# Kernel optimization log

Hardware: AMD Instinct MI355X
Metric: run time of the kernel (lower is better)

## Reference

```python
import jax, jax.numpy as jnp
import numpy as np

B, T, D, L = 16, 2048, 1024, 4


def setup_inputs() -> dict:
    key = jax.random.key(0)
    k1, k2, k3 = jax.random.split(key, 3)
    x = jax.random.normal(k1, (B, T, D), dtype=jnp.float32)
    lengths = jax.random.randint(k2, (B,), 1, T + 1, dtype=jnp.int32)
    s = float(np.sqrt(3.0 / D))  # SRU uniform init range
    W = jax.random.uniform(k3, (L, D, 3 * D), dtype=jnp.float32, minval=-s, maxval=s)
    b = jnp.zeros((L, 2 * D), dtype=jnp.float32)
    return {"x": x, "lengths": lengths, "W": W, "b": b}


def _sru_layer(h, W_l, b_l):
    # h: [T, B, D]; W_l: [D, 3D]; b_l: [2D]
    U = jnp.einsum('tbd,de->tbe', h, W_l)            # [T, B, 3D]
    x_tilde, zf, zr = jnp.split(U, 3, axis=-1)
    f = jax.nn.sigmoid(zf + b_l[:D])                 # forget gate
    r = jax.nn.sigmoid(zr + b_l[D:])                 # reset/highway gate

    def step(c, fx):
        f_t, x_t = fx
        c_new = f_t * c + (1.0 - f_t) * x_t          # c_t = f*c_{t-1} + (1-f)*x~
        return c_new, c_new

    c0 = jnp.zeros(h.shape[1:], dtype=h.dtype)       # [B, D]
    _, c_seq = jax.lax.scan(step, c0, (f, x_tilde))  # [T, B, D]
    # v1 + has_skip_term, n_in == n_out: highway over raw input
    return r * jnp.tanh(c_seq) + (1.0 - r) * h


def reference(x, lengths, W, b):
    # x: [B, T, D] -> [T, B, D] (module permutes before SRU)
    h = jnp.transpose(x, (1, 0, 2))
    for l in range(L):  # fixed small layer count
        h = _sru_layer(h, W[l], b[l])
    h = jnp.transpose(h, (1, 0, 2))                  # [B, T, D]
    # _select_last: pick h[i, lengths[i]-1]
    return h[jnp.arange(B), lengths - 1]             # [B, D]
```

## Files before the change

kernel.cpp:

```cpp
#include <hip/hip_runtime.h>


typedef float f32x4 __attribute__((ext_vector_type(4)));
typedef int   i32x4 __attribute__((ext_vector_type(4)));
typedef char  c8x4  __attribute__((ext_vector_type(4)));
typedef _Float16 f16;

#define SRU_B 16
#define SRU_T 2048
#define SRU_D 1024
#define SRU_L 4
#define SRU_N 3072
#define SPAN 256

#define A_SCALE 4096.0f
#define W_SCALE 2048.0f
#define Z2_INV  1.1920928955078125e-7f
#define H_INV   2.44140625e-4f

__device__ __forceinline__ void q16split(float v, float scale, signed char& hi,
                                         signed char& lo) {
  int q = __float2int_rn(v * scale);
  q = min(max(q, -32512), 32512);
  int h = (q + 128) >> 8;
  hi = (signed char)h;
  lo = (signed char)(q - (h << 8));
}

__device__ __forceinline__ void mfma_i8(i32x4& c, i32x4 a, i32x4 b) {
  asm("v_mfma_i32_16x16x64_i8 %0, %1, %2, %0" : "+v"(c) : "v"(a), "v"(b));
}

#define GLDS(g, l) __builtin_amdgcn_global_load_lds(                      \
    (const __attribute__((address_space(1))) void*)(g),                   \
    (__attribute__((address_space(3))) void*)(l), 16, 0, 0)

__global__ void convert_w_kernel(const float* __restrict__ W,
                                 signed char* __restrict__ Wt8) {
  __shared__ float tile[32][33];
  const int l = blockIdx.z;
  const int n0 = blockIdx.x * 32, k0 = blockIdx.y * 32;
  const int tx = threadIdx.x & 31, ty = threadIdx.x >> 5;
  const float* Wl = W + (size_t)l * SRU_D * SRU_N;
#pragma unroll
  for (int i = 0; i < 32; i += 8)
    tile[ty + i][tx] = Wl[(size_t)(k0 + ty + i) * SRU_N + n0 + tx];
  __syncthreads();
  const size_t ob = (size_t)l * SRU_N * SRU_D;
#pragma unroll
  for (int i = 0; i < 32; i += 8) {
    float v = tile[tx][ty + i];
    size_t o = ob + (size_t)(n0 + ty + i) * SRU_D + k0 + tx;
    Wt8[o] = (signed char)__float2int_rn(v * W_SCALE);
  }
}

__global__ void convert_x_kernel(const float* __restrict__ x,
                                 const int* __restrict__ lengths,
                                 signed char* __restrict__ Hh,
                                 signed char* __restrict__ Hl) {
  const size_t i = (size_t)blockIdx.x * 256 + threadIdx.x;
  const int b = (int)(i >> 19), t = (int)((i >> 8) & 2047);
  if (t >= lengths[b]) return;
  f32x4 v = ((const f32x4*)x)[i];
  c8x4 hi, lo;
#pragma unroll
  for (int j = 0; j < 4; ++j) {
    signed char h, l;
    q16split(v[j], A_SCALE, h, l);
    hi[j] = h;
    lo[j] = l;
  }
  ((c8x4*)Hh)[i] = hi;
  ((c8x4*)Hl)[i] = lo;
}

__global__ __launch_bounds__(256, 2) void gemm2_kernel(
    const signed char* __restrict__ Ah, const signed char* __restrict__ Al,
    const signed char* __restrict__ Bq,
    const int* __restrict__ lengths, const float* __restrict__ bias,
    f16* __restrict__ Ux, f16* __restrict__ Uf, f16* __restrict__ Ur,
    int last) {
  const int bn = blockIdx.x, bm = blockIdx.y;
  const int b = bm >> 4, tb = bm & 15;
  const int lenb = lengths[b];
  if (tb * 128 >= lenb) return;
  if (last && bn >= 16) {
    if (((lenb - 1) >> 7) != tb) return;
  }

  __shared__ __align__(16) signed char lAh[16384], lAl[16384], lB[16384];
  const int tid = threadIdx.x;
  const int lane = tid & 63, wid = tid >> 6;
  const int wm = (wid >> 1) * 64, wn = (wid & 1) * 64;
  const int fr = lane & 15;
  const int fko = ((lane >> 4) * 16) ^ (((lane >> 1) & 3) * 16);

  i32x4 acc1[4][4] = {};
  i32x4 acc2[4][4] = {};

  const int sr = tid >> 2;
  const int sc = (((tid & 3) ^ ((tid >> 3) & 3)) * 16);
  const size_t abase = ((size_t)b * SRU_T + tb * 128) * SRU_D;
  const signed char* gAh = Ah + abase + (size_t)sr * 1024 + sc;
  const signed char* gAl = Al + abase + (size_t)sr * 1024 + sc;
  const signed char* gB  = Bq + (size_t)(bn * 128 + sr) * 1024 + sc;

  auto stage = [&](int k0, int bs) {
    const int o = bs * 8192 + wid * 1024;
    GLDS(gAh + k0, &lAh[o]); GLDS(gAh + 65536 + k0, &lAh[o + 4096]);
    GLDS(gAl + k0, &lAl[o]); GLDS(gAl + 65536 + k0, &lAl[o + 4096]);
    GLDS(gB  + k0, &lB[o]);  GLDS(gB  + 65536 + k0, &lB[o + 4096]);
  };

  stage(0, 0);
  __syncthreads();
  int cur = 0;
  for (int step = 0; step < 16; ++step) {
    if (step + 1 < 16) stage((step + 1) * 64, cur ^ 1);
    const int cb = cur * 8192;
    i32x4 ah[4], al[4];
#pragma unroll
    for (int i = 0; i < 4; ++i) {
      const int ro = cb + (wm + i * 16 + fr) * 64 + fko;
      ah[i] = *(const i32x4*)&lAh[ro];
      al[i] = *(const i32x4*)&lAl[ro];
    }
#pragma unroll
    for (int ni = 0; ni < 4; ++ni) {
      const int ro = cb + (wn + ni * 16 + fr) * 64 + fko;
      i32x4 bv = *(const i32x4*)&lB[ro];
#pragma unroll
      for (int mi = 0; mi < 4; ++mi) {
        mfma_i8(acc1[mi][ni], ah[mi], bv);
        mfma_i8(acc2[mi][ni], al[mi], bv);
      }
    }
    __syncthreads();
    cur ^= 1;
  }

  const int urow0 = bm * 128 + wm + (lane >> 4) * 4;
  const int gcol = bn * 128 + wn + fr;
  const int region = gcol >> 10;
  const int d0 = gcol & 1023;
  if (region == 0) {
#pragma unroll
    for (int mi = 0; mi < 4; ++mi)
#pragma unroll
      for (int ni = 0; ni < 4; ++ni)
#pragma unroll
        for (int r = 0; r < 4; ++r) {
          float z = (256.f * (float)acc1[mi][ni][r] +
                     (float)acc2[mi][ni][r]) * Z2_INV;
          Ux[((size_t)(urow0 + mi * 16 + r) << 10) + d0 + ni * 16] = (f16)z;
        }
  } else {
    const float* bp = bias + (region == 2 ? SRU_D : 0);
    float bv[4];
#pragma unroll
    for (int ni = 0; ni < 4; ++ni) bv[ni] = bp[d0 + ni * 16];
    f16* dst = (region == 1) ? Uf : Ur;
#pragma unroll
    for (int mi = 0; mi < 4; ++mi)
#pragma unroll
      for (int ni = 0; ni < 4; ++ni)
#pragma unroll
        for (int r = 0; r < 4; ++r) {
          float z = (256.f * (float)acc1[mi][ni][r] +
                     (float)acc2[mi][ni][r]) * Z2_INV;
          float s = 1.f / (1.f + __expf(-(z + bv[ni])));
          dst[((size_t)(urow0 + mi * 16 + r) << 10) + d0 + ni * 16] = (f16)s;
        }
  }
}

__global__ __launch_bounds__(512) void scan_kernel(
    const f16* __restrict__ Ux, const f16* __restrict__ Uf,
    const f16* __restrict__ Ur,
    const int* __restrict__ lengths,
    signed char* __restrict__ Hh, signed char* __restrict__ Hl, int last) {
  __shared__ float sP[8][64], sL[8][64];
  const int dblk = blockIdx.x, b = blockIdx.y;
  const int lane = threadIdx.x & 63, w = threadIdx.x >> 6;
  const int d = (dblk << 6) + lane;
  const int lenb = lengths[b];
  const int start = w * SPAN;
  const size_t rbase = (((size_t)b * SRU_T + start) << 10) + d;

  float P = 1.f, Lv = 0.f;
  if (start < lenb) {
    const int nbt = (min(SPAN, lenb - start) + 7) >> 3;
    const f16* Xr = Ux + rbase;
    const f16* Fr = Uf + rbase;
    float xt_n[8], ff_n[8];
#pragma unroll
    for (int j = 0; j < 8; ++j) {
      xt_n[j] = (float)Xr[(size_t)j << 10];
      ff_n[j] = (float)Fr[(size_t)j << 10];
    }
    for (int bt = 0; bt < nbt; ++bt) {
      float xt[8], ff[8];
#pragma unroll
      for (int j = 0; j < 8; ++j) { xt[j] = xt_n[j]; ff[j] = ff_n[j]; }
      if (bt + 1 < nbt) {
        const size_t o2 = (size_t)((bt + 1) * 8) << 10;
#pragma unroll
        for (int j = 0; j < 8; ++j) {
          xt_n[j] = (float)Xr[o2 + ((size_t)j << 10)];
          ff_n[j] = (float)Fr[o2 + ((size_t)j << 10)];
        }
      }
#pragma unroll
      for (int j = 0; j < 8; ++j) {
        Lv = ff[j] * Lv + (1.f - ff[j]) * xt[j];
        P *= ff[j];
      }
    }
  }
  sP[w][lane] = P;
  sL[w][lane] = Lv;
  __syncthreads();
  if (start >= lenb) return;

  float c = 0.f;
#pragma unroll
  for (int j = 0; j < 8; ++j)
    if (j < w) c = sP[j][lane] * c + sL[j][lane];

  const int nbt = (min(SPAN, lenb - start) + 7) >> 3;
  const f16* Xr = Ux + rbase;
  const f16* Fr = Uf + rbase;
  const f16* Rr = Ur + rbase;
  signed char* ph = Hh + rbase;
  signed char* pl = Hl + rbase;

  float xt_n[8], ff_n[8], rr_n[8], hv_n[8];
#pragma unroll
  for (int j = 0; j < 8; ++j) {
    xt_n[j] = (float)Xr[(size_t)j << 10];
    ff_n[j] = (float)Fr[(size_t)j << 10];
    rr_n[j] = (float)Rr[(size_t)j << 10];
    hv_n[j] = (float)((int)ph[(size_t)j << 10] * 256 + (int)pl[(size_t)j << 10]) * H_INV;
  }
  for (int bt = 0; bt < nbt; ++bt) {
    float xt[8], ff[8], rr[8], hv[8];
#pragma unroll
    for (int j = 0; j < 8; ++j) {
      xt[j] = xt_n[j]; ff[j] = ff_n[j]; rr[j] = rr_n[j]; hv[j] = hv_n[j];
    }
    if (bt + 1 < nbt) {
      const size_t o2 = (size_t)((bt + 1) * 8) << 10;
#pragma unroll
      for (int j = 0; j < 8; ++j) {
        xt_n[j] = (float)Xr[o2 + ((size_t)j << 10)];
        ff_n[j] = (float)Fr[o2 + ((size_t)j << 10)];
        rr_n[j] = (float)Rr[o2 + ((size_t)j << 10)];
        hv_n[j] = (float)((int)ph[o2 + ((size_t)j << 10)] * 256 +
                          (int)pl[o2 + ((size_t)j << 10)]) * H_INV;
      }
    }
    signed char* wh = ph + ((size_t)(bt * 8) << 10);
    signed char* wl = pl + ((size_t)(bt * 8) << 10);
#pragma unroll
    for (int j = 0; j < 8; ++j) {
      c = ff[j] * c + (1.f - ff[j]) * xt[j];
      const int t = start + bt * 8 + j;
      const bool wr = last ? (t == lenb - 1) : (t < lenb);
      if (wr) {
        float e = __expf(-2.f * fabsf(c));
        float th = copysignf((1.f - e) / (1.f + e), c);
        float o = rr[j] * th + (1.f - rr[j]) * hv[j];
        signed char oh, ol;
        q16split(o, A_SCALE, oh, ol);
        wh[(size_t)j << 10] = oh;
        wl[(size_t)j << 10] = ol;
      }
    }
  }
}

__global__ void select_kernel(const signed char* __restrict__ Hh,
                              const signed char* __restrict__ Hl,
                              const int* __restrict__ lengths,
                              float* __restrict__ out) {
  const int b = blockIdx.x;
  const int t = lengths[b] - 1;
#pragma unroll
  for (int j = 0; j < 4; ++j) {
    int d = threadIdx.x + j * 256;
    size_t idx = (((size_t)b * SRU_T + t) << 10) + d;
    out[(b << 10) + d] = (float)((int)Hh[idx] * 256 + (int)Hl[idx]) * H_INV;
  }
}

extern "C" void kernel_launch(void* const* d_in, const int* in_sizes, int n_in,
                              void* d_out, int out_size, void* d_ws, size_t ws_size,
                              hipStream_t stream) {
  const float* x = (const float*)d_in[0];
  const int* lengths = (const int*)d_in[1];
  const float* W = (const float*)d_in[2];
  const float* bias = (const float*)d_in[3];
  float* out = (float*)d_out;

  char* ws = (char*)d_ws;
  size_t off = 0;
  auto alloc = [&](size_t n) { void* p = ws + off; off += (n + 255) & ~(size_t)255; return p; };
  signed char* Hh  = (signed char*)alloc((size_t)SRU_T * SRU_B * SRU_D);
  signed char* Hl  = (signed char*)alloc((size_t)SRU_T * SRU_B * SRU_D);
  signed char* Wt8 = (signed char*)alloc((size_t)SRU_L * SRU_N * SRU_D);
  f16*   Ux   = (f16*)alloc((size_t)SRU_T * SRU_B * SRU_D * 2);
  f16*   Uf   = (f16*)alloc((size_t)SRU_T * SRU_B * SRU_D * 2);
  f16*   Ur   = (f16*)alloc((size_t)SRU_T * SRU_B * SRU_D * 2);

  hipLaunchKernelGGL(convert_w_kernel, dim3(SRU_N / 32, SRU_D / 32, SRU_L), dim3(256), 0, stream,
                     W, Wt8);
  hipLaunchKernelGGL(convert_x_kernel, dim3((SRU_B * SRU_T * SRU_D / 4) / 256), dim3(256), 0, stream,
                     x, lengths, Hh, Hl);

  for (int l = 0; l < SRU_L; ++l) {
    const signed char* Bq = Wt8 + (size_t)l * SRU_N * SRU_D;
    const float* bl_ = bias + (size_t)l * 2 * SRU_D;
    const int last = (l == SRU_L - 1) ? 1 : 0;
    hipLaunchKernelGGL(gemm2_kernel, dim3(SRU_N / 128, SRU_B * SRU_T / 128), dim3(256), 0, stream,
                       Hh, Hl, Bq, lengths, bl_, Ux, Uf, Ur, last);
    hipLaunchKernelGGL(scan_kernel, dim3(SRU_D / 64, SRU_B), dim3(512), 0, stream,
                       Ux, Uf, Ur, lengths, Hh, Hl, last);
  }
  hipLaunchKernelGGL(select_kernel, dim3(SRU_B), dim3(256), 0, stream, Hh, Hl, lengths, out);
}
```

Measured before the change: 889.0 us.

## Remap GEMM blocks across XCDs and fold final selection into last scan

```diff
diff --git a/kernel.cpp b/kernel.cpp
--- a/kernel.cpp
+++ b/kernel.cpp
@@ -81,13 +81,19 @@
     const int* __restrict__ lengths, const float* __restrict__ bias,
     f16* __restrict__ Ux, f16* __restrict__ Uf, f16* __restrict__ Ur,
     int last) {
-  const int bn = blockIdx.x, bm = blockIdx.y;
-  const int b = bm >> 4, tb = bm & 15;
+  const int id = blockIdx.x;
+  const int xcd = id & 7;
+  const int r = id >> 3;
+  const int bn = r % 24;
+  const int q = r / 24;
+  const int b = q >> 1;
+  const int tb = ((xcd - b) & 7) | ((q & 1) << 3);
   const int lenb = lengths[b];
   if (tb * 128 >= lenb) return;
   if (last && bn >= 16) {
     if (((lenb - 1) >> 7) != tb) return;
   }
+  const int bm = (b << 4) | tb;
 
   __shared__ __align__(16) signed char lAh[16384], lAl[16384], lB[16384];
   const int tid = threadIdx.x;
@@ -150,10 +156,10 @@
 #pragma unroll
       for (int ni = 0; ni < 4; ++ni)
 #pragma unroll
-        for (int r = 0; r < 4; ++r) {
-          float z = (256.f * (float)acc1[mi][ni][r] +
-                     (float)acc2[mi][ni][r]) * Z2_INV;
-          Ux[((size_t)(urow0 + mi * 16 + r) << 10) + d0 + ni * 16] = (f16)z;
+        for (int r2 = 0; r2 < 4; ++r2) {
+          float z = (256.f * (float)acc1[mi][ni][r2] +
+                     (float)acc2[mi][ni][r2]) * Z2_INV;
+          Ux[((size_t)(urow0 + mi * 16 + r2) << 10) + d0 + ni * 16] = (f16)z;
         }
   } else {
     const float* bp = bias + (region == 2 ? SRU_D : 0);
@@ -166,11 +172,11 @@
 #pragma unroll
       for (int ni = 0; ni < 4; ++ni)
 #pragma unroll
-        for (int r = 0; r < 4; ++r) {
-          float z = (256.f * (float)acc1[mi][ni][r] +
-                     (float)acc2[mi][ni][r]) * Z2_INV;
+        for (int r2 = 0; r2 < 4; ++r2) {
+          float z = (256.f * (float)acc1[mi][ni][r2] +
+                     (float)acc2[mi][ni][r2]) * Z2_INV;
           float s = 1.f / (1.f + __expf(-(z + bv[ni])));
-          dst[((size_t)(urow0 + mi * 16 + r) << 10) + d0 + ni * 16] = (f16)s;
+          dst[((size_t)(urow0 + mi * 16 + r2) << 10) + d0 + ni * 16] = (f16)s;
         }
   }
 }
@@ -179,7 +185,8 @@
     const f16* __restrict__ Ux, const f16* __restrict__ Uf,
     const f16* __restrict__ Ur,
     const int* __restrict__ lengths,
-    signed char* __restrict__ Hh, signed char* __restrict__ Hl, int last) {
+    signed char* __restrict__ Hh, signed char* __restrict__ Hl,
+    float* __restrict__ out, int last) {
   __shared__ float sP[8][64], sL[8][64];
   const int dblk = blockIdx.x, b = blockIdx.y;
   const int lane = threadIdx.x & 63, w = threadIdx.x >> 6;
@@ -222,6 +229,7 @@
   sL[w][lane] = Lv;
   __syncthreads();
   if (start >= lenb) return;
+  if (last && (lenb - 1 < start || lenb - 1 >= start + SPAN)) return;
 
   float c = 0.f;
 #pragma unroll
@@ -266,8 +274,13 @@
     for (int j = 0; j < 8; ++j) {
       c = ff[j] * c + (1.f - ff[j]) * xt[j];
       const int t = start + bt * 8 + j;
-      const bool wr = last ? (t == lenb - 1) : (t < lenb);
-      if (wr) {
+      if (last) {
+        if (t == lenb - 1) {
+          float e = __expf(-2.f * fabsf(c));
+          float th = copysignf((1.f - e) / (1.f + e), c);
+          out[(b << 10) + d] = rr[j] * th + (1.f - rr[j]) * hv[j];
+        }
+      } else if (t < lenb) {
         float e = __expf(-2.f * fabsf(c));
         float th = copysignf((1.f - e) / (1.f + e), c);
         float o = rr[j] * th + (1.f - rr[j]) * hv[j];
@@ -277,20 +290,6 @@
         wl[(size_t)j << 10] = ol;
       }
     }
-  }
-}
-
-__global__ void select_kernel(const signed char* __restrict__ Hh,
-                              const signed char* __restrict__ Hl,
-                              const int* __restrict__ lengths,
-                              float* __restrict__ out) {
-  const int b = blockIdx.x;
-  const int t = lengths[b] - 1;
-#pragma unroll
-  for (int j = 0; j < 4; ++j) {
-    int d = threadIdx.x + j * 256;
-    size_t idx = (((size_t)b * SRU_T + t) << 10) + d;
-    out[(b << 10) + d] = (float)((int)Hh[idx] * 256 + (int)Hl[idx]) * H_INV;
   }
 }
 
@@ -322,10 +321,9 @@
     const signed char* Bq = Wt8 + (size_t)l * SRU_N * SRU_D;
     const float* bl_ = bias + (size_t)l * 2 * SRU_D;
     const int last = (l == SRU_L - 1) ? 1 : 0;
-    hipLaunchKernelGGL(gemm2_kernel, dim3(SRU_N / 128, SRU_B * SRU_T / 128), dim3(256), 0, stream,
+    hipLaunchKernelGGL(gemm2_kernel, dim3(24 * 256), dim3(256), 0, stream,
                        Hh, Hl, Bq, lengths, bl_, Ux, Uf, Ur, last);
     hipLaunchKernelGGL(scan_kernel, dim3(SRU_D / 64, SRU_B), dim3(512), 0, stream,
-                       Ux, Uf, Ur, lengths, Hh, Hl, last);
-  }
-  hipLaunchKernelGGL(select_kernel, dim3(SRU_B), dim3(256), 0, stream, Hh, Hl, lengths, out);
-}
+                       Ux, Uf, Ur, lengths, Hh, Hl, out, last);
+  }
+}
```

After: 866.9 us. 2.5% less time.
